# Kernel tuning notes

Measured on AMD Instinct MI355X. Metric: run time of the kernel, lower is better.

Reference implementation:

```python
import jax, jax.numpy as jnp
import numpy as np

N_LAYERS = 2  # BasicEntanglerLayers depth of the qlayer surrogate
N_WIRES = 4
CNOT_RING = [(0, 1), (1, 2), (2, 3), (3, 0)]


def _ry(state, q, theta):
    # state: (N, 2, 2, 2, 2) real statevector; RY is a real 2x2 rotation.
    N = state.shape[0]
    theta = jnp.broadcast_to(jnp.asarray(theta, state.dtype), (N,)).reshape(N, 1, 1, 1)
    c, s = jnp.cos(theta * 0.5), jnp.sin(theta * 0.5)
    s0 = jax.lax.index_in_dim(state, 0, q + 1, keepdims=False)  # (N,2,2,2)
    s1 = jax.lax.index_in_dim(state, 1, q + 1, keepdims=False)
    return jnp.stack([c * s0 - s * s1, s * s0 + c * s1], axis=q + 1)


def _cnot(state, c, t):
    # flip target axis on the control=1 slab
    s0 = jax.lax.index_in_dim(state, 0, c + 1, keepdims=True)
    s1 = jax.lax.index_in_dim(state, 1, c + 1, keepdims=True)
    return jnp.concatenate([s0, jnp.flip(s1, axis=t + 1)], axis=c + 1)


def _qcircuit(xblk, qweights):
    # xblk: (N, 4) embedding angles; qweights: (L, 4). Returns expval Z0, shape (N,).
    N = xblk.shape[0]
    state = jnp.zeros((N, 2, 2, 2, 2), xblk.dtype).at[:, 0, 0, 0, 0].set(1.0)
    for i in range(N_WIRES):                      # AngleEmbedding (RY)
        state = _ry(state, i, xblk[:, i])
    for l in range(N_LAYERS):                     # BasicEntanglerLayers
        for i in range(N_WIRES):
            state = _ry(state, i, qweights[l, i])
        for c, t in CNOT_RING:
            state = _cnot(state, c, t)
    p = state * state
    return p[:, 0].sum(axis=(1, 2, 3)) - p[:, 1].sum(axis=(1, 2, 3))


def _filtering(x):
    # (B, 784) -> (B*14*14, 4): 2x2 blocks of the 28x28 image
    B = x.shape[0]
    return x.reshape(B, 14, 2, 14, 2).transpose(0, 1, 3, 2, 4).reshape(B * 196, 4)


def setup_inputs() -> dict:
    key = jax.random.key(0)
    ks = jax.random.split(key, 6)
    B = 4096
    return {
        "x": jax.random.uniform(ks[0], (B, 784), jnp.float32),
        "qweights": jax.random.normal(ks[1], (N_LAYERS, N_WIRES), jnp.float32),
        "W1": jax.random.normal(ks[2], (196, 30), jnp.float32) * (1.0 / np.sqrt(196)),
        "b1": jax.random.normal(ks[3], (30,), jnp.float32) * 0.01,
        "W2": jax.random.normal(ks[4], (30, 2), jnp.float32) * (1.0 / np.sqrt(30)),
        "b2": jax.random.normal(ks[5], (2,), jnp.float32) * 0.01,
    }


def reference(x, qweights, W1, b1, W2, b2):
    B = x.shape[0]
    blocks = _filtering(x)                 # (B*196, 4)
    z = _qcircuit(blocks, qweights)        # (B*196,) — batched over all blocks
    h = z.reshape(B, 196)
    h = jnp.maximum(h @ W1 + b1, 0.0)      # Linear(196,30) + ReLU
    return h @ W2 + b2                     # Linear(30,2)
```

## Files before the change

kernel.cpp:

```cpp
#include <hip/hip_runtime.h>


__global__ __launch_bounds__(256) void hybrid_qnn_kernel(
    const float* __restrict__ x,
    const float* __restrict__ qw,
    const float* __restrict__ W1,
    const float* __restrict__ b1,
    const float* __restrict__ W2,
    const float* __restrict__ b2,
    float* __restrict__ out)
{
    __shared__ float lz[196];
    __shared__ float lh[30];

    const int img = blockIdx.x;
    const int t   = threadIdx.x;

    if (t < 196) {
        const int i = t / 14;
        const int j = t - 14 * i;
        const float* xp = x + (size_t)img * 784 + i * 56 + j * 2;
        const float2 r0 = *(const float2*)xp;
        const float2 r1 = *(const float2*)(xp + 28);

        float c0,s0,c1,s1,c2,s2,c3,s3;
        __sincosf(0.5f * (r0.x + qw[0]), &s0, &c0);
        __sincosf(0.5f * (r0.y + qw[1]), &s1, &c1);
        __sincosf(0.5f * (r1.x + qw[2]), &s2, &c2);
        __sincosf(0.5f * (r1.y + qw[3]), &s3, &c3);

        float cw[4], sw[4];
        #pragma unroll
        for (int k = 0; k < 4; ++k)
            __sincosf(0.5f * qw[4 + k], &sw[k], &cw[k]);

        float st[16];
        {
            float f01[4] = {c0*c1, c0*s1, s0*c1, s0*s1};
            float f23[4] = {c2*c3, c2*s3, s2*c3, s2*s3};
            #pragma unroll
            for (int a = 0; a < 4; ++a)
                #pragma unroll
                for (int b = 0; b < 4; ++b)
                    st[a*4+b] = f01[a] * f23[b];
        }

#define RY_GATE(MASK, C, S) { \
        _Pragma("unroll") \
        for (int idx = 0; idx < 16; ++idx) { \
            if (!(idx & (MASK))) { \
                float u0 = st[idx], u1 = st[idx | (MASK)]; \
                st[idx]          = (C)*u0 - (S)*u1; \
                st[idx | (MASK)] = (S)*u0 + (C)*u1; \
            } \
        } }

#define CNOT_GATE(CM, TM) { \
        _Pragma("unroll") \
        for (int idx = 0; idx < 16; ++idx) { \
            if ((idx & (CM)) && !(idx & (TM))) { \
                float tmp = st[idx]; st[idx] = st[idx | (TM)]; st[idx | (TM)] = tmp; \
            } \
        } }

        CNOT_GATE(8, 4);
        CNOT_GATE(4, 2);
        CNOT_GATE(2, 1);
        CNOT_GATE(1, 8);
        RY_GATE(8, cw[0], sw[0]);
        RY_GATE(4, cw[1], sw[1]);
        RY_GATE(2, cw[2], sw[2]);
        RY_GATE(1, cw[3], sw[3]);
        CNOT_GATE(8, 4);
        CNOT_GATE(4, 2);
        CNOT_GATE(2, 1);
        CNOT_GATE(1, 8);
#undef RY_GATE
#undef CNOT_GATE

        float zp = 0.f, zn = 0.f;
        #pragma unroll
        for (int idx = 0; idx < 8; ++idx)  zp = fmaf(st[idx], st[idx], zp);
        #pragma unroll
        for (int idx = 8; idx < 16; ++idx) zn = fmaf(st[idx], st[idx], zn);
        lz[t] = zp - zn;
    }
    __syncthreads();

    if (t < 240) {
        const int o   = t >> 3;
        const int seg = t & 7;
        float acc = 0.f;
        #pragma unroll
        for (int i = 0; i < 25; ++i) {
            const int j = seg * 25 + i;
            if (j < 196) acc = fmaf(lz[j], W1[j * 30 + o], acc);
        }
        acc += __shfl_down(acc, 4, 8);
        acc += __shfl_down(acc, 2, 8);
        acc += __shfl_down(acc, 1, 8);
        if (seg == 0) lh[o] = fmaxf(acc + b1[o], 0.f);
    }
    __syncthreads();

    if (t < 2) {
        float acc = b2[t];
        #pragma unroll
        for (int k = 0; k < 30; ++k)
            acc = fmaf(lh[k], W2[k * 2 + t], acc);
        out[img * 2 + t] = acc;
    }
}

extern "C" void kernel_launch(void* const* d_in, const int* in_sizes, int n_in,
                              void* d_out, int out_size, void* d_ws, size_t ws_size,
                              hipStream_t stream) {
    const float* x  = (const float*)d_in[0];
    const float* qw = (const float*)d_in[1];
    const float* W1 = (const float*)d_in[2];
    const float* b1 = (const float*)d_in[3];
    const float* W2 = (const float*)d_in[4];
    const float* b2 = (const float*)d_in[5];
    float* out = (float*)d_out;

    const int B = in_sizes[0] / 784;
    hipLaunchKernelGGL(hybrid_qnn_kernel, dim3(B), dim3(256), 0, stream,
                       x, qw, W1, b1, W2, b2, out);
}
```

Baseline: 84.53 us.

## Precompute observable tensor from weights and evaluate expectation as trig polynomial

A small pre-kernel builds the circuit unitary from the weight layer, forms the Heisenberg-picture observable U^T Z0 U, and projects it onto per-qubit {1, cos a, sin a} bases into an 81-entry tensor T stored in workspace. The main kernel then evaluates each block's expectation as a nested multilinear contraction with cos/sin of the full angles, replacing the per-thread 16-amplitude statevector simulation. This trades per-thread gate arithmetic and registers for a second launch and 81 scalar reads of T per thread, which should hit cache.

```diff
diff --git a/kernel.cpp b/kernel.cpp
--- a/kernel.cpp
+++ b/kernel.cpp
@@ -1,9 +1,86 @@
 #include <hip/hip_runtime.h>
 
+
+#define CNOT_GATE(CM, TM) { \
+    _Pragma("unroll") \
+    for (int idx = 0; idx < 16; ++idx) { \
+        if ((idx & (CM)) && !(idx & (TM))) { \
+            float tmp = st[idx]; st[idx] = st[idx | (TM)]; st[idx | (TM)] = tmp; \
+        } \
+    } }
+
+#define RY_GATE(MASK, C, S) { \
+    _Pragma("unroll") \
+    for (int idx = 0; idx < 16; ++idx) { \
+        if (!(idx & (MASK))) { \
+            float u0 = st[idx], u1 = st[idx | (MASK)]; \
+            st[idx]          = (C)*u0 - (S)*u1; \
+            st[idx | (MASK)] = (S)*u0 + (C)*u1; \
+        } \
+    } }
+
+__device__ __forceinline__ float gval(int p, int a, int b) {
+    if (p == 0) return (a == b) ? 0.5f : 0.0f;
+    if (p == 1) return (a == b) ? (a ? -0.5f : 0.5f) : 0.0f;
+    return (a != b) ? 0.5f : 0.0f;
+}
+
+__global__ __launch_bounds__(256) void precompute_T_kernel(
+    const float* __restrict__ qw, float* __restrict__ T)
+{
+    __shared__ float U[16][16];
+    __shared__ float M[16][16];
+    const int t = threadIdx.x;
+
+    if (t < 16) {
+        float st[16];
+        #pragma unroll
+        for (int k = 0; k < 16; ++k) st[k] = (k == t) ? 1.0f : 0.0f;
+        CNOT_GATE(8, 4); CNOT_GATE(4, 2); CNOT_GATE(2, 1); CNOT_GATE(1, 8);
+        float cw[4], sw[4];
+        #pragma unroll
+        for (int w = 0; w < 4; ++w) {
+            cw[w] = cosf(0.5f * qw[4 + w]);
+            sw[w] = sinf(0.5f * qw[4 + w]);
+        }
+        RY_GATE(8, cw[0], sw[0]);
+        RY_GATE(4, cw[1], sw[1]);
+        RY_GATE(2, cw[2], sw[2]);
+        RY_GATE(1, cw[3], sw[3]);
+        CNOT_GATE(8, 4); CNOT_GATE(4, 2); CNOT_GATE(2, 1); CNOT_GATE(1, 8);
+        #pragma unroll
+        for (int k = 0; k < 16; ++k) U[k][t] = st[k];
+    }
+    __syncthreads();
+    {
+        const int i = t >> 4, j = t & 15;
+        float m = 0.f;
+        #pragma unroll
+        for (int k = 0; k < 16; ++k)
+            m = fmaf((k < 8 ? 1.0f : -1.0f) * U[k][i], U[k][j], m);
+        M[i][j] = m;
+    }
+    __syncthreads();
+    if (t < 81) {
+        const int p0 = t / 27, p1 = (t / 9) % 3, p2 = (t / 3) % 3, p3 = t % 3;
+        float acc = 0.f;
+        for (int i = 0; i < 16; ++i) {
+            for (int j = 0; j < 16; ++j) {
+                const float w = gval(p0, (i >> 3) & 1, (j >> 3) & 1)
+                              * gval(p1, (i >> 2) & 1, (j >> 2) & 1)
+                              * gval(p2, (i >> 1) & 1, (j >> 1) & 1)
+                              * gval(p3, i & 1, j & 1);
+                if (w != 0.f) acc = fmaf(w, M[i][j], acc);
+            }
+        }
+        T[t] = acc;
+    }
+}
 
 __global__ __launch_bounds__(256) void hybrid_qnn_kernel(
     const float* __restrict__ x,
     const float* __restrict__ qw,
+    const float* __restrict__ T,
     const float* __restrict__ W1,
     const float* __restrict__ b1,
     const float* __restrict__ W2,
@@ -23,67 +100,37 @@
         const float2 r0 = *(const float2*)xp;
         const float2 r1 = *(const float2*)(xp + 28);
 
-        float c0,s0,c1,s1,c2,s2,c3,s3;
-        __sincosf(0.5f * (r0.x + qw[0]), &s0, &c0);
-        __sincosf(0.5f * (r0.y + qw[1]), &s1, &c1);
-        __sincosf(0.5f * (r1.x + qw[2]), &s2, &c2);
-        __sincosf(0.5f * (r1.y + qw[3]), &s3, &c3);
+        const float a0 = r0.x + qw[0];
+        const float a1 = r0.y + qw[1];
+        const float a2 = r1.x + qw[2];
+        const float a3 = r1.y + qw[3];
+        const float C0 = __cosf(a0), S0 = __sinf(a0);
+        const float C1 = __cosf(a1), S1 = __sinf(a1);
+        const float C2 = __cosf(a2), S2 = __sinf(a2);
+        const float C3 = __cosf(a3), S3 = __sinf(a3);
 
-        float cw[4], sw[4];
+        const float e0[3] = {1.f, C0, S0};
+        const float e1[3] = {1.f, C1, S1};
+        const float e2[3] = {1.f, C2, S2};
+
+        float z = 0.f;
         #pragma unroll
-        for (int k = 0; k < 4; ++k)
-            __sincosf(0.5f * qw[4 + k], &sw[k], &cw[k]);
-
-        float st[16];
-        {
-            float f01[4] = {c0*c1, c0*s1, s0*c1, s0*s1};
-            float f23[4] = {c2*c3, c2*s3, s2*c3, s2*s3};
+        for (int p0 = 0; p0 < 3; ++p0) {
+            float s1 = 0.f;
             #pragma unroll
-            for (int a = 0; a < 4; ++a)
+            for (int p1 = 0; p1 < 3; ++p1) {
+                float s2 = 0.f;
                 #pragma unroll
-                for (int b = 0; b < 4; ++b)
-                    st[a*4+b] = f01[a] * f23[b];
+                for (int p2 = 0; p2 < 3; ++p2) {
+                    const int b = ((p0 * 3 + p1) * 3 + p2) * 3;
+                    float s3 = fmaf(S3, T[b + 2], fmaf(C3, T[b + 1], T[b]));
+                    s2 = fmaf(s3, e2[p2], s2);
+                }
+                s1 = fmaf(s2, e1[p1], s1);
+            }
+            z = fmaf(s1, e0[p0], z);
         }
-
-#define RY_GATE(MASK, C, S) { \
-        _Pragma("unroll") \
-        for (int idx = 0; idx < 16; ++idx) { \
-            if (!(idx & (MASK))) { \
-                float u0 = st[idx], u1 = st[idx | (MASK)]; \
-                st[idx]          = (C)*u0 - (S)*u1; \
-                st[idx | (MASK)] = (S)*u0 + (C)*u1; \
-            } \
-        } }
-
-#define CNOT_GATE(CM, TM) { \
-        _Pragma("unroll") \
-        for (int idx = 0; idx < 16; ++idx) { \
-            if ((idx & (CM)) && !(idx & (TM))) { \
-                float tmp = st[idx]; st[idx] = st[idx | (TM)]; st[idx | (TM)] = tmp; \
-            } \
-        } }
-
-        CNOT_GATE(8, 4);
-        CNOT_GATE(4, 2);
-        CNOT_GATE(2, 1);
-        CNOT_GATE(1, 8);
-        RY_GATE(8, cw[0], sw[0]);
-        RY_GATE(4, cw[1], sw[1]);
-        RY_GATE(2, cw[2], sw[2]);
-        RY_GATE(1, cw[3], sw[3]);
-        CNOT_GATE(8, 4);
-        CNOT_GATE(4, 2);
-        CNOT_GATE(2, 1);
-        CNOT_GATE(1, 8);
-#undef RY_GATE
-#undef CNOT_GATE
-
-        float zp = 0.f, zn = 0.f;
-        #pragma unroll
-        for (int idx = 0; idx < 8; ++idx)  zp = fmaf(st[idx], st[idx], zp);
-        #pragma unroll
-        for (int idx = 8; idx < 16; ++idx) zn = fmaf(st[idx], st[idx], zn);
-        lz[t] = zp - zn;
+        lz[t] = z;
     }
     __syncthreads();
 
@@ -122,8 +169,10 @@
     const float* W2 = (const float*)d_in[4];
     const float* b2 = (const float*)d_in[5];
     float* out = (float*)d_out;
+    float* T   = (float*)d_ws;
 
     const int B = in_sizes[0] / 784;
+    hipLaunchKernelGGL(precompute_T_kernel, dim3(1), dim3(256), 0, stream, qw, T);
     hipLaunchKernelGGL(hybrid_qnn_kernel, dim3(B), dim3(256), 0, stream,
-                       x, qw, W1, b1, W2, b2, out);
+                       x, qw, T, W1, b1, W2, b2, out);
 }
```

Result: slower. 148.7 us (+75.9%).

## Replace statevector simulation with closed-form expectation value

Applied to the files above, without the earlier changes.

Replaces the 16-amplitude statevector simulation (product state, CNOT and RY gates, squared-amplitude reduction) with an analytic closed-form expression for <Z0> built from cosines and sines of the full angles. Half-angle sincos calls become full-angle cos/sin, and the first-layer weight qw[4] drops out. This removes many register-resident FMAs per thread. The risks are that the derived formula is wrong for general inputs and that the fast trig intrinsics lose accuracy.

```diff
diff --git a/kernel.cpp b/kernel.cpp
--- a/kernel.cpp
+++ b/kernel.cpp
@@ -23,67 +23,25 @@
         const float2 r0 = *(const float2*)xp;
         const float2 r1 = *(const float2*)(xp + 28);
 
-        float c0,s0,c1,s1,c2,s2,c3,s3;
-        __sincosf(0.5f * (r0.x + qw[0]), &s0, &c0);
-        __sincosf(0.5f * (r0.y + qw[1]), &s1, &c1);
-        __sincosf(0.5f * (r1.x + qw[2]), &s2, &c2);
-        __sincosf(0.5f * (r1.y + qw[3]), &s3, &c3);
+        const float a0 = r0.x + qw[0];
+        const float a1 = r0.y + qw[1];
+        const float a2 = r1.x + qw[2];
+        const float a3 = r1.y + qw[3];
+        const float C0 = __cosf(a0), S0 = __sinf(a0);
+        const float C1 = __cosf(a1), S1 = __sinf(a1);
+        const float C2 = __cosf(a2), S2 = __sinf(a2);
+        const float C3 = __cosf(a3), S3 = __sinf(a3);
 
-        float cw[4], sw[4];
-        #pragma unroll
-        for (int k = 0; k < 4; ++k)
-            __sincosf(0.5f * qw[4 + k], &sw[k], &cw[k]);
+        const float c1 = __cosf(qw[5]), s1 = __sinf(qw[5]);
+        const float c2 = __cosf(qw[6]), s2 = __sinf(qw[6]);
+        const float c3 = __cosf(qw[7]), s3 = __sinf(qw[7]);
 
-        float st[16];
-        {
-            float f01[4] = {c0*c1, c0*s1, s0*c1, s0*s1};
-            float f23[4] = {c2*c3, c2*s3, s2*c3, s2*s3};
-            #pragma unroll
-            for (int a = 0; a < 4; ++a)
-                #pragma unroll
-                for (int b = 0; b < 4; ++b)
-                    st[a*4+b] = f01[a] * f23[b];
-        }
-
-#define RY_GATE(MASK, C, S) { \
-        _Pragma("unroll") \
-        for (int idx = 0; idx < 16; ++idx) { \
-            if (!(idx & (MASK))) { \
-                float u0 = st[idx], u1 = st[idx | (MASK)]; \
-                st[idx]          = (C)*u0 - (S)*u1; \
-                st[idx | (MASK)] = (S)*u0 + (C)*u1; \
-            } \
-        } }
-
-#define CNOT_GATE(CM, TM) { \
-        _Pragma("unroll") \
-        for (int idx = 0; idx < 16; ++idx) { \
-            if ((idx & (CM)) && !(idx & (TM))) { \
-                float tmp = st[idx]; st[idx] = st[idx | (TM)]; st[idx | (TM)] = tmp; \
-            } \
-        } }
-
-        CNOT_GATE(8, 4);
-        CNOT_GATE(4, 2);
-        CNOT_GATE(2, 1);
-        CNOT_GATE(1, 8);
-        RY_GATE(8, cw[0], sw[0]);
-        RY_GATE(4, cw[1], sw[1]);
-        RY_GATE(2, cw[2], sw[2]);
-        RY_GATE(1, cw[3], sw[3]);
-        CNOT_GATE(8, 4);
-        CNOT_GATE(4, 2);
-        CNOT_GATE(2, 1);
-        CNOT_GATE(1, 8);
-#undef RY_GATE
-#undef CNOT_GATE
-
-        float zp = 0.f, zn = 0.f;
-        #pragma unroll
-        for (int idx = 0; idx < 8; ++idx)  zp = fmaf(st[idx], st[idx], zp);
-        #pragma unroll
-        for (int idx = 8; idx < 16; ++idx) zn = fmaf(st[idx], st[idx], zn);
-        lz[t] = zp - zn;
+        const float c1c2 = c1 * c2;
+        float z =        (c1c2 * c3) * (C0 * C1 * C3);
+        z = fmaf(-(c1c2 * s3), (S0 * S1) * (C2 * S3), z);
+        z = fmaf(-(s1 * c2 * c3), (S1 * S2) * C3, z);
+        z = fmaf(-(s1 * s2 * s3), S0, z);
+        lz[t] = z;
     }
     __syncthreads();
 
```

After: 84.04 us. About the same (-0.6%).
